# Performance work log

Measured on AMD Instinct MI355X. Metric: run time of the kernel, lower is better.

Reference implementation:

```python
import jax, jax.numpy as jnp
import numpy as np

EMBED_DIM = 512

def _eq_linear(x, W):
    # EqualizedLinear: weight scaled by 1/sqrt(fan_in), no bias.
    c = 1.0 / np.sqrt(W.shape[1])
    return jnp.einsum('bnd,ed->bne', x, W) * c

def setup_inputs() -> dict:
    key = jax.random.key(0)
    ks = jax.random.split(key, 6)
    b, n, d = 8, 2048, 512
    return {
        'q': jax.random.normal(ks[0], (b, n, d), jnp.float32),
        'k': jax.random.normal(ks[1], (b, n, d), jnp.float32),
        'v': jax.random.normal(ks[2], (b, n, d), jnp.float32),
        'Wq': jax.random.normal(ks[3], (EMBED_DIM, d), jnp.float32),
        'Wk': jax.random.normal(ks[4], (EMBED_DIM, d), jnp.float32),
        'Wv': jax.random.normal(ks[5], (EMBED_DIM, d), jnp.float32),
    }

def reference(q, k, v, Wq, Wk, Wv):
    scale = EMBED_DIM ** (-0.5)
    qp = _eq_linear(q, Wq)  # [b, n, e]
    kp = _eq_linear(k, Wk)  # [b, m, e]
    vp = _eq_linear(v, Wv)  # [b, m, e]
    dots = jnp.einsum('bne,bme->bnm', qp, kp) * scale
    attn = jax.nn.softmax(dots, axis=-1)
    out = jnp.einsum('bnm,bme->bne', attn, vp)
    return (out, (jax.lax.stop_gradient(attn),))
```

## Files before the change

kernel.cpp:

```cpp
#include <hip/hip_runtime.h>
#include <math.h>

constexpr int BATCH = 8;
constexpr int SEQ   = 2048;
constexpr int DIM   = 512;

typedef _Float16 f16x8  __attribute__((ext_vector_type(8)));
typedef float    f32x4  __attribute__((ext_vector_type(4)));
typedef float    f32x16 __attribute__((ext_vector_type(16)));

__device__ __forceinline__ void gload_lds16(const void* g, void* l) {
    __builtin_amdgcn_global_load_lds(
        (const __attribute__((address_space(1))) void*)g,
        (__attribute__((address_space(3))) void*)l, 16, 0, 0);
}

template<bool OUT_F16>
__global__ __launch_bounds__(256, 3) void gemm_nt_f16(
    const _Float16* __restrict__ A, int lda, long sA,
    const _Float16* __restrict__ B, int ldb, long sB,
    void* __restrict__ Cv, int ldc, long sC,
    int K, float alpha)
{
    __shared__ _Float16 As[8][128][8];
    __shared__ _Float16 Bs[8][128][8];

    int lin = blockIdx.x + gridDim.x * (blockIdx.y + gridDim.y * blockIdx.z);
    const int nwg = gridDim.x * gridDim.y * gridDim.z;
    lin = (lin & 7) * (nwg >> 3) + (lin >> 3);
    const int bx  = lin % gridDim.x;
    const int byz = lin / gridDim.x;
    const int by  = byz % gridDim.y;
    const int bz  = byz / gridDim.y;

    A += (long)bz * sA;  B += (long)bz * sB;
    const long bm = (long)by * 128;
    const long bn = (long)bx * 128;
    const int t    = threadIdx.x;
    const int lane = t & 63;
    const int wave = t >> 6;
    const int wm = (wave >> 1) * 64;
    const int wn = (wave & 1) * 64;
    const int ml = lane & 31;
    const int kh = lane >> 5;

    f32x16 acc[2][2] = {};

    for (int k0 = 0; k0 < K; k0 += 64) {
#pragma unroll
        for (int s = 0; s < 4; s++) {
            const int idx = wave * 4 + s;
            const int ch  = idx >> 1;
            const int r0  = (idx & 1) * 64;
            const _Float16* gp = A + (bm + r0 + lane) * (long)lda + k0 + ch * 8;
            gload_lds16(gp, &As[ch][r0][0]);
        }
#pragma unroll
        for (int s = 0; s < 4; s++) {
            const int idx = wave * 4 + s;
            const int ch  = idx >> 1;
            const int r0  = (idx & 1) * 64;
            const _Float16* gp = B + (bn + r0 + lane) * (long)ldb + k0 + ch * 8;
            gload_lds16(gp, &Bs[ch][r0][0]);
        }
        __syncthreads();

#pragma unroll
        for (int ks = 0; ks < 4; ks++) {
            const int ch = ks * 2 + kh;
            f16x8 a0 = *(const f16x8*)&As[ch][wm      + ml][0];
            f16x8 a1 = *(const f16x8*)&As[ch][wm + 32 + ml][0];
            f16x8 b0 = *(const f16x8*)&Bs[ch][wn      + ml][0];
            f16x8 b1 = *(const f16x8*)&Bs[ch][wn + 32 + ml][0];
            acc[0][0] = __builtin_amdgcn_mfma_f32_32x32x16_f16(a0, b0, acc[0][0], 0, 0, 0);
            acc[0][1] = __builtin_amdgcn_mfma_f32_32x32x16_f16(a0, b1, acc[0][1], 0, 0, 0);
            acc[1][0] = __builtin_amdgcn_mfma_f32_32x32x16_f16(a1, b0, acc[1][0], 0, 0, 0);
            acc[1][1] = __builtin_amdgcn_mfma_f32_32x32x16_f16(a1, b1, acc[1][1], 0, 0, 0);
        }
        __syncthreads();
    }

    float*    Cf = (float*)Cv    + (OUT_F16 ? 0 : (long)bz * sC);
    _Float16* Ch = (_Float16*)Cv + (OUT_F16 ? (long)bz * sC : 0);
#pragma unroll
    for (int i = 0; i < 2; i++)
#pragma unroll
        for (int j = 0; j < 2; j++) {
            const long col = bn + wn + j * 32 + ml;
#pragma unroll
            for (int rg = 0; rg < 16; rg++) {
                const long row = bm + wm + i * 32 + (rg & 3) + 8 * (rg >> 2) + 4 * kh;
                if constexpr (OUT_F16)
                    Ch[row * (long)ldc + col] = (_Float16)(alpha * acc[i][j][rg]);
                else
                    __builtin_nontemporal_store(alpha * acc[i][j][rg],
                                                &Cf[row * (long)ldc + col]);
            }
        }
}

__global__ __launch_bounds__(256) void gemm_tn_f32(
    const float* __restrict__ A, int lda,
    const float* __restrict__ B, int ldb,
    _Float16* __restrict__ C, int ldc, int K, float alpha)
{
    __shared__ float As[16][68];
    __shared__ float Bs[16][68];
    const int bm = blockIdx.y * 64;
    const int bn = blockIdx.x * 64;
    const int t  = threadIdx.x;
    const int tx = t & 15, ty = t >> 4;
    const int kk = t >> 4, mc = (t & 15) * 4;

    float acc[4][4] = {};
    for (int k0 = 0; k0 < K; k0 += 16) {
        float4 a = *(const float4*)(A + (long)(k0 + kk) * lda + bm + mc);
        float4 b = *(const float4*)(B + (long)(k0 + kk) * ldb + bn + mc);
        __syncthreads();
        As[kk][mc] = a.x; As[kk][mc + 1] = a.y; As[kk][mc + 2] = a.z; As[kk][mc + 3] = a.w;
        Bs[kk][mc] = b.x; Bs[kk][mc + 1] = b.y; Bs[kk][mc + 2] = b.z; Bs[kk][mc + 3] = b.w;
        __syncthreads();
#pragma unroll
        for (int k = 0; k < 16; k++) {
            float ar[4], br[4];
#pragma unroll
            for (int i = 0; i < 4; i++) ar[i] = As[k][ty * 4 + i];
#pragma unroll
            for (int j = 0; j < 4; j++) br[j] = Bs[k][tx * 4 + j];
#pragma unroll
            for (int i = 0; i < 4; i++)
#pragma unroll
                for (int j = 0; j < 4; j++) acc[i][j] = fmaf(ar[i], br[j], acc[i][j]);
        }
    }
#pragma unroll
    for (int i = 0; i < 4; i++)
#pragma unroll
        for (int j = 0; j < 4; j++)
            C[(long)(bm + ty * 4 + i) * ldc + bn + tx * 4 + j] =
                (_Float16)(alpha * acc[i][j]);
}

__global__ __launch_bounds__(256) void softmax_rows(
    _Float16* __restrict__ dots, float* __restrict__ attn)
{
    const long row = blockIdx.x;
    _Float16* ph = dots + row * (long)SEQ + threadIdx.x * 8;
    float*    pf = attn + row * (long)SEQ + threadIdx.x * 8;
    const int t = threadIdx.x;

    f16x8 h = *(const f16x8*)ph;
    float x[8];
#pragma unroll
    for (int i = 0; i < 8; i++) x[i] = (float)h[i];

    float m = x[0];
#pragma unroll
    for (int i = 1; i < 8; i++) m = fmaxf(m, x[i]);
#pragma unroll
    for (int off = 32; off > 0; off >>= 1) m = fmaxf(m, __shfl_xor(m, off));
    __shared__ float sm[4];
    __shared__ float ss[4];
    const int wave = t >> 6;
    if ((t & 63) == 0) sm[wave] = m;
    __syncthreads();
    m = fmaxf(fmaxf(sm[0], sm[1]), fmaxf(sm[2], sm[3]));

    float s = 0.0f;
#pragma unroll
    for (int i = 0; i < 8; i++) { x[i] = __expf(x[i] - m); s += x[i]; }
#pragma unroll
    for (int off = 32; off > 0; off >>= 1) s += __shfl_xor(s, off);
    if ((t & 63) == 0) ss[wave] = s;
    __syncthreads();
    s = ss[0] + ss[1] + ss[2] + ss[3];
    const float inv = 1.0f / s;

    f32x4 o0, o1;
    o0[0] = x[0] * inv; o0[1] = x[1] * inv; o0[2] = x[2] * inv; o0[3] = x[3] * inv;
    o1[0] = x[4] * inv; o1[1] = x[5] * inv; o1[2] = x[6] * inv; o1[3] = x[7] * inv;
    f32x4* pv = (f32x4*)pf;
    __builtin_nontemporal_store(o0, pv);
    __builtin_nontemporal_store(o1, pv + 1);

    f16x8 hn;
    hn[0] = (_Float16)o0[0]; hn[1] = (_Float16)o0[1];
    hn[2] = (_Float16)o0[2]; hn[3] = (_Float16)o0[3];
    hn[4] = (_Float16)o1[0]; hn[5] = (_Float16)o1[1];
    hn[6] = (_Float16)o1[2]; hn[7] = (_Float16)o1[3];
    *(f16x8*)ph = hn;
}

__global__ __launch_bounds__(256) void conv_all(
    const float* __restrict__ q, const float* __restrict__ k,
    const float* __restrict__ v, const float* __restrict__ Wv,
    _Float16* __restrict__ q16, _Float16* __restrict__ k16,
    _Float16* __restrict__ v16, _Float16* __restrict__ Wv16)
{
    int i = blockIdx.x * 256 + threadIdx.x;
    const float* src; _Float16* dst;
    if (i < 1048576)      { src = q;  dst = q16; }
    else if (i < 2097152) { src = k;  dst = k16;  i -= 1048576; }
    else if (i < 3145728) { src = v;  dst = v16;  i -= 2097152; }
    else                  { src = Wv; dst = Wv16; i -= 3145728; }
    const float4 a = ((const float4*)src)[2 * i];
    const float4 b = ((const float4*)src)[2 * i + 1];
    f16x8 h;
    h[0] = (_Float16)a.x; h[1] = (_Float16)a.y; h[2] = (_Float16)a.z; h[3] = (_Float16)a.w;
    h[4] = (_Float16)b.x; h[5] = (_Float16)b.y; h[6] = (_Float16)b.z; h[7] = (_Float16)b.w;
    ((f16x8*)dst)[i] = h;
}

extern "C" void kernel_launch(void* const* d_in, const int* in_sizes, int n_in,
                              void* d_out, int out_size, void* d_ws, size_t ws_size,
                              hipStream_t stream)
{
    const float* q  = (const float*)d_in[0];
    const float* k  = (const float*)d_in[1];
    const float* v  = (const float*)d_in[2];
    const float* Wq = (const float*)d_in[3];
    const float* Wk = (const float*)d_in[4];
    const float* Wv = (const float*)d_in[5];

    float* out  = (float*)d_out;
    float* attn = (float*)d_out + (size_t)BATCH * SEQ * DIM;

    char* w = (char*)d_ws;
    _Float16* q16    = (_Float16*)(w);
    _Float16* dots16 = (_Float16*)(w);
    _Float16* k16    = (_Float16*)(w + 67108864);
    _Float16* v16    = (_Float16*)(w + 83886080);
    _Float16* T16    = (_Float16*)(w + 100663296);
    _Float16* vpT16  = (_Float16*)(w + 117440512);
    _Float16* Wv16   = (_Float16*)(w + 134217728);
    _Float16* P16    = (_Float16*)(w + 134742016);

    const float c = 0.044194173824159216f;

    conv_all<<<dim3(12416), 256, 0, stream>>>(q, k, v, Wv, q16, k16, v16, Wv16);

    gemm_tn_f32<<<dim3(8, 8), 256, 0, stream>>>(Wk, DIM, Wq, DIM, P16, DIM, DIM, c * c);

    gemm_nt_f16<true><<<dim3(4, 128, 1), 256, 0, stream>>>(
        q16, DIM, 0, P16, DIM, 0, T16, DIM, 0, DIM, 1.0f);

    gemm_nt_f16<true><<<dim3(16, 16, 8), 256, 0, stream>>>(
        T16, DIM, (long)SEQ * DIM, k16, DIM, (long)SEQ * DIM,
        dots16, SEQ, (long)SEQ * SEQ, DIM, c);

    gemm_nt_f16<true><<<dim3(16, 4, 8), 256, 0, stream>>>(
        Wv16, DIM, 0, v16, DIM, (long)SEQ * DIM,
        vpT16, SEQ, (long)DIM * SEQ, DIM, c);

    softmax_rows<<<dim3(BATCH * SEQ), 256, 0, stream>>>(dots16, attn);

    gemm_nt_f16<false><<<dim3(4, 16, 8), 256, 0, stream>>>(
        dots16, SEQ, (long)SEQ * SEQ, vpT16, SEQ, (long)DIM * SEQ,
        out, DIM, (long)SEQ * DIM, SEQ, 1.0f);
}
```

Measured before the change: 494.9 us.

## Split-K the weight-product GEMM, raise GEMM occupancy, use nontemporal loads in conversion

Splits the small Wk^T·Wq fp32 GEMM across 8 K-slices (512 blocks instead of 64) and adds a reduction kernel that sums the partials, applies the scale and writes fp16. This is meant to fill the GPU on a launch that previously used very few workgroups, at the cost of an extra launch and 8 MB of partial traffic. It also vectorizes the LDS reads in that GEMM, raises the f16 GEMM launch bound from 3 to 4 waves per SIMD, and uses nontemporal loads in the input conversion kernel. The higher occupancy hint may force register spills.

```diff
diff --git a/kernel.cpp b/kernel.cpp
--- a/kernel.cpp
+++ b/kernel.cpp
@@ -16,7 +16,7 @@
 }
 
 template<bool OUT_F16>
-__global__ __launch_bounds__(256, 3) void gemm_nt_f16(
+__global__ __launch_bounds__(256, 4) void gemm_nt_f16(
     const _Float16* __restrict__ A, int lda, long sA,
     const _Float16* __restrict__ B, int ldb, long sB,
     void* __restrict__ Cv, int ldc, long sC,
@@ -99,21 +99,22 @@
         }
 }
 
-__global__ __launch_bounds__(256) void gemm_tn_f32(
+__global__ __launch_bounds__(256) void gemm_tn_f32_sk(
     const float* __restrict__ A, int lda,
     const float* __restrict__ B, int ldb,
-    _Float16* __restrict__ C, int ldc, int K, float alpha)
+    float* __restrict__ Cpart, int ldc)
 {
     __shared__ float As[16][68];
     __shared__ float Bs[16][68];
     const int bm = blockIdx.y * 64;
     const int bn = blockIdx.x * 64;
+    const int kb = blockIdx.z * 64;
     const int t  = threadIdx.x;
     const int tx = t & 15, ty = t >> 4;
     const int kk = t >> 4, mc = (t & 15) * 4;
 
     float acc[4][4] = {};
-    for (int k0 = 0; k0 < K; k0 += 16) {
+    for (int k0 = kb; k0 < kb + 64; k0 += 16) {
         float4 a = *(const float4*)(A + (long)(k0 + kk) * lda + bm + mc);
         float4 b = *(const float4*)(B + (long)(k0 + kk) * ldb + bn + mc);
         __syncthreads();
@@ -122,23 +123,30 @@
         __syncthreads();
 #pragma unroll
         for (int k = 0; k < 16; k++) {
-            float ar[4], br[4];
-#pragma unroll
-            for (int i = 0; i < 4; i++) ar[i] = As[k][ty * 4 + i];
-#pragma unroll
-            for (int j = 0; j < 4; j++) br[j] = Bs[k][tx * 4 + j];
+            f32x4 ar = *(const f32x4*)&As[k][ty * 4];
+            f32x4 br = *(const f32x4*)&Bs[k][tx * 4];
 #pragma unroll
             for (int i = 0; i < 4; i++)
 #pragma unroll
                 for (int j = 0; j < 4; j++) acc[i][j] = fmaf(ar[i], br[j], acc[i][j]);
         }
     }
+    float* Cp = Cpart + (long)blockIdx.z * DIM * DIM;
 #pragma unroll
     for (int i = 0; i < 4; i++)
 #pragma unroll
         for (int j = 0; j < 4; j++)
-            C[(long)(bm + ty * 4 + i) * ldc + bn + tx * 4 + j] =
-                (_Float16)(alpha * acc[i][j]);
+            Cp[(long)(bm + ty * 4 + i) * ldc + bn + tx * 4 + j] = acc[i][j];
+}
+
+__global__ __launch_bounds__(256) void reduce_p(
+    const float* __restrict__ Cpart, _Float16* __restrict__ P, float alpha)
+{
+    const int idx = blockIdx.x * 256 + threadIdx.x;
+    float s = 0.0f;
+#pragma unroll
+    for (int sl = 0; sl < 8; sl++) s += Cpart[(long)sl * DIM * DIM + idx];
+    P[idx] = (_Float16)(alpha * s);
 }
 
 __global__ __launch_bounds__(256) void softmax_rows(
@@ -203,11 +211,11 @@
     else if (i < 2097152) { src = k;  dst = k16;  i -= 1048576; }
     else if (i < 3145728) { src = v;  dst = v16;  i -= 2097152; }
     else                  { src = Wv; dst = Wv16; i -= 3145728; }
-    const float4 a = ((const float4*)src)[2 * i];
-    const float4 b = ((const float4*)src)[2 * i + 1];
+    const f32x4 a = __builtin_nontemporal_load((const f32x4*)src + 2 * i);
+    const f32x4 b = __builtin_nontemporal_load((const f32x4*)src + 2 * i + 1);
     f16x8 h;
-    h[0] = (_Float16)a.x; h[1] = (_Float16)a.y; h[2] = (_Float16)a.z; h[3] = (_Float16)a.w;
-    h[4] = (_Float16)b.x; h[5] = (_Float16)b.y; h[6] = (_Float16)b.z; h[7] = (_Float16)b.w;
+    h[0] = (_Float16)a[0]; h[1] = (_Float16)a[1]; h[2] = (_Float16)a[2]; h[3] = (_Float16)a[3];
+    h[4] = (_Float16)b[0]; h[5] = (_Float16)b[1]; h[6] = (_Float16)b[2]; h[7] = (_Float16)b[3];
     ((f16x8*)dst)[i] = h;
 }
 
@@ -234,12 +242,14 @@
     _Float16* vpT16  = (_Float16*)(w + 117440512);
     _Float16* Wv16   = (_Float16*)(w + 134217728);
     _Float16* P16    = (_Float16*)(w + 134742016);
+    float*    Ppart  = (float*)   (w + 201326592);
 
     const float c = 0.044194173824159216f;
 
     conv_all<<<dim3(12416), 256, 0, stream>>>(q, k, v, Wv, q16, k16, v16, Wv16);
 
-    gemm_tn_f32<<<dim3(8, 8), 256, 0, stream>>>(Wk, DIM, Wq, DIM, P16, DIM, DIM, c * c);
+    gemm_tn_f32_sk<<<dim3(8, 8, 8), 256, 0, stream>>>(Wk, DIM, Wq, DIM, Ppart, DIM);
+    reduce_p<<<dim3(1024), 256, 0, stream>>>(Ppart, P16, c * c);
 
     gemm_nt_f16<true><<<dim3(4, 128, 1), 256, 0, stream>>>(
         q16, DIM, 0, P16, DIM, 0, T16, DIM, 0, DIM, 1.0f);
```

Measured after the change: 462.6 us. -6.5%, faster.
